# Kernel tuning notes

Hardware: AMD Instinct MI355X
Metric: run time of the kernel (lower is better)

Reference implementation:

```python
import jax, jax.numpy as jnp
import numpy as np

LOG_2PI = float(np.log(2.0 * np.pi))
LOSS_BETA = 1.0
SIGMA = 1.0
EPS = 1e-6


def setup_inputs() -> dict:
    key = jax.random.key(0)
    z_activations = jax.random.normal(key, (2048, 16, 8), dtype=jnp.float32)
    return {"z_activations": z_activations}


def reference(z_activations):
    N, num_attr, pose_dim = z_activations.shape
    x = z_activations.reshape(N, -1)  # (N, K)
    K = x.shape[1]

    # standardize (torch.std is unbiased, ddof=1)
    mean = jnp.mean(x, axis=0, keepdims=True)
    std = jnp.std(x, axis=0, keepdims=True, ddof=1)
    x = (x - mean) / (std + EPS)

    logN = jnp.log(jnp.asarray(N, dtype=x.dtype))

    # per-dimension pairwise squared differences: (N, N, K)
    d = (x[:, None, :] - x[None, :, :]) ** 2

    # joint: log p(x_i | x_j) for K-dim Gaussian, sigma=1
    sq_dist = jnp.sum(d, axis=2)  # (N, N)
    c_joint = -0.5 * K * LOG_2PI - K * jnp.log(jnp.asarray(SIGMA, dtype=x.dtype))
    log_prob_joint = c_joint - sq_dist / (2.0 * SIGMA ** 2)
    log_q_z_given_x = jax.nn.logsumexp(log_prob_joint, axis=1) - logN  # (N,)

    # marginals: 1-D Gaussian per dim, all K at once (fuses the torch K-loop)
    c_marg = -0.5 * LOG_2PI - jnp.log(jnp.asarray(SIGMA, dtype=x.dtype))
    log_prob_marg = c_marg - d / (2.0 * SIGMA ** 2)  # (N, N, K)
    log_q_z_j = jax.nn.logsumexp(log_prob_marg, axis=1) - logN  # (N, K)
    sum_log_q_z_j = jnp.sum(log_q_z_j, axis=1)  # (N,)

    tc_loss = jnp.mean(log_q_z_given_x - sum_log_q_z_j)
    return tc_loss * LOSS_BETA
```

## Files before the change

kernel.cpp:

```cpp
#include <hip/hip_runtime.h>
#include <hip/hip_bf16.h>

#define NROWS 2048
#define KDIM  128
#define NCELL 16
#define PORD  10
#define NJBLK 512

typedef float f32x4  __attribute__((ext_vector_type(4)));
typedef short bf16x8 __attribute__((ext_vector_type(8)));

__device__ __forceinline__ float fexp2(float x){ return __builtin_amdgcn_exp2f(x); }
__device__ __forceinline__ float flog2(float x){ return __builtin_amdgcn_logf(x); }

#define CS 0.8493218002880191f

#define OFF_PART   0
#define OFF_ACCUM  8192
#define OFF_JOINT  8448
#define OFF_SLOG   10496
#define OFF_MOM    12544
#define OFF_CTR    33024
#define OFF_XS     33028
#define ZERO_BASE  OFF_JOINT
#define ZERO_LEN   (2048 + 2048 + 20480 + 4)

__device__ __forceinline__ void col_stats_from(float s, float s2, float& scale, float& shift){
  float m = s * (1.f / NROWS);
  float var = fmaxf((s2 - (float)NROWS * m * m) * (1.f / (NROWS - 1)), 0.f);
  scale = 1.f / (sqrtf(var) + 1e-6f);
  shift = -m * scale;
}

__global__ __launch_bounds__(1024) void tc_stats(const float* __restrict__ x,
                                                 float* __restrict__ ws){
  const int t  = threadIdx.x;
  const int k  = t & 127;
  const int rg = t >> 7;
  const int r0 = blockIdx.x * 64;
  {
    int idx = blockIdx.x * 1024 + t;
    if (idx < ZERO_LEN) ws[ZERO_BASE + idx] = 0.f;
  }
  float s = 0.f, s2 = 0.f;
  #pragma unroll
  for (int it = 0; it < 8; ++it){
    float v = x[(size_t)(r0 + it * 8 + rg) * KDIM + k];
    s += v;
    s2 = fmaf(v, v, s2);
  }
  __shared__ float ls[8][128], ls2[8][128];
  ls[rg][k] = s; ls2[rg][k] = s2;
  __syncthreads();
  if (t < 128){
    float a = 0.f, b = 0.f;
    #pragma unroll
    for (int g = 0; g < 8; ++g){ a += ls[g][t]; b += ls2[g][t]; }
    ws[OFF_PART + blockIdx.x * 256 + t]       = a;
    ws[OFF_PART + blockIdx.x * 256 + 128 + t] = b;
  }
}

__global__ __launch_bounds__(128) void tc_moments(const float* __restrict__ x,
                                                  float* __restrict__ ws){
  const int k   = blockIdx.x >> 4;
  const int seg = blockIdx.x & 15;
  const int t   = threadIdx.x;
  __shared__ float lm[NCELL * PORD];
  lm[t] = 0.f;
  if (t < 32) lm[128 + t] = 0.f;

  float s = 0.f, s2 = 0.f;
  #pragma unroll
  for (int b = 0; b < 32; ++b){
    s  += ws[OFF_PART + b * 256 + k];
    s2 += ws[OFF_PART + b * 256 + 128 + k];
  }
  if (seg == 0 && t == 0){
    ws[OFF_ACCUM + k]       = s;
    ws[OFF_ACCUM + 128 + k] = s2;
  }
  float scale, shift; col_stats_from(s, s2, scale, shift);
  __syncthreads();

  const int row = seg * 128 + t;
  float y = fmaf(x[(size_t)row * KDIM + k], scale, shift);

  {
    __hip_bfloat16 hb = __float2bfloat16(y * CS);
    ((unsigned short*)(ws + OFF_XS))[(size_t)row * KDIM + k] = *(unsigned short*)&hb;
  }

  int c = (int)floorf(y * 2.f + 8.f);
  c = min(max(c, 0), NCELL - 1);
  float u = y - (-3.75f + 0.5f * (float)c);
  float* b10 = &lm[c * PORD];
  atomicAdd(&b10[0], 1.f);
  float pw = u;
  atomicAdd(&b10[1], pw);
  pw *= u; atomicAdd(&b10[2], pw * 0.5f);
  pw *= u; atomicAdd(&b10[3], pw * 1.6666666666e-1f);
  pw *= u; atomicAdd(&b10[4], pw * 4.1666666666e-2f);
  pw *= u; atomicAdd(&b10[5], pw * 8.3333333333e-3f);
  pw *= u; atomicAdd(&b10[6], pw * 1.3888888889e-3f);
  pw *= u; atomicAdd(&b10[7], pw * 1.9841269841e-4f);
  pw *= u; atomicAdd(&b10[8], pw * 2.4801587302e-5f);
  pw *= u; atomicAdd(&b10[9], pw * 2.7557319224e-6f);
  __syncthreads();

  float* mom = ws + OFF_MOM;
  for (int idx = t; idx < NCELL * PORD; idx += 128){
    int c2 = idx / PORD, m = idx - c2 * PORD;
    atomicAdd(&mom[(size_t)(c2 * KDIM + k) * PORD + m], lm[idx]);
  }
}

__global__ __launch_bounds__(512) void tc_joint(const float* __restrict__ x,
                                                float* __restrict__ ws,
                                                float* __restrict__ out){
  __shared__ __align__(16) char ls[49152];
  __shared__ float nI[128], nJ[64];
  __shared__ float red2[8];
  __shared__ int lastflag;

  const int t = threadIdx.x;
  const int wave = t >> 6, lane = t & 63;
  const int bid = blockIdx.x;
  const int bi = bid >> 5, bj = bid & 31;
  const int Ibase = bi * 128, Jbase = bj * 64;
  float* joint = ws + OFF_JOINT;
  float* slog  = ws + OFF_SLOG;
  const float* accum = ws + OFF_ACCUM;
  const float* mom   = ws + OFF_MOM;
  const unsigned short* xs = (const unsigned short*)(ws + OFF_XS);

  #pragma unroll
  for (int q = 0; q < 4; ++q){
    int g = t + q * 512;
    int row = g >> 4, c16 = g & 15;
    uint4 v = *(const uint4*)(xs + (size_t)(Ibase + row) * KDIM + c16 * 8);
    *(uint4*)(ls + row * 256 + ((c16 * 16) ^ ((row & 7) << 4))) = v;
  }
  #pragma unroll
  for (int q = 0; q < 2; ++q){
    int g = t + q * 512;
    int row = g >> 4, c16 = g & 15;
    uint4 v = *(const uint4*)(xs + (size_t)(Jbase + row) * KDIM + c16 * 8);
    *(uint4*)(ls + 32768 + row * 256 + ((c16 * 16) ^ ((row & 7) << 4))) = v;
  }
  __syncthreads();

  if (t < 192){
    int row = (t < 128) ? t : (t - 128);
    const char* base = (t < 128) ? ls : (ls + 32768);
    float n = 0.f;
    #pragma unroll
    for (int g2 = 0; g2 < 16; ++g2){
      uint4 v = *(const uint4*)(base + row * 256 + ((g2 * 16) ^ ((row & 7) << 4)));
      const unsigned int* u = (const unsigned int*)&v;
      #pragma unroll
      for (int e = 0; e < 4; ++e){
        float lo = __builtin_bit_cast(float, u[e] << 16);
        float hi = __builtin_bit_cast(float, u[e] & 0xFFFF0000u);
        n = fmaf(lo, lo, n); n = fmaf(hi, hi, n);
      }
    }
    if (t < 128) nI[row] = n; else nJ[row] = n;
  }
  __syncthreads();

  const int wi = wave >> 2, wj = wave & 3;
  const int mrow0 = wi * 64 + (lane & 15);
  const int nrow  = wj * 16 + (lane & 15);
  f32x4 acc0 = {0.f,0.f,0.f,0.f}, acc1 = acc0, acc2 = acc0, acc3 = acc0;
  #pragma unroll
  for (int kq = 0; kq < 4; ++kq){
    const int boff = kq * 64 + (lane >> 4) * 16;
    const int mx = (mrow0 & 7) << 4;
    bf16x8 bf = *(const bf16x8*)(ls + 32768 + nrow * 256 + (boff ^ ((nrow & 7) << 4)));
    bf16x8 a0 = *(const bf16x8*)(ls + (mrow0 +  0) * 256 + (boff ^ mx));
    bf16x8 a1 = *(const bf16x8*)(ls + (mrow0 + 16) * 256 + (boff ^ mx));
    bf16x8 a2 = *(const bf16x8*)(ls + (mrow0 + 32) * 256 + (boff ^ mx));
    bf16x8 a3 = *(const bf16x8*)(ls + (mrow0 + 48) * 256 + (boff ^ mx));
    acc0 = __builtin_amdgcn_mfma_f32_16x16x32_bf16(a0, bf, acc0, 0, 0, 0);
    acc1 = __builtin_amdgcn_mfma_f32_16x16x32_bf16(a1, bf, acc1, 0, 0, 0);
    acc2 = __builtin_amdgcn_mfma_f32_16x16x32_bf16(a2, bf, acc2, 0, 0, 0);
    acc3 = __builtin_amdgcn_mfma_f32_16x16x32_bf16(a3, bf, acc3, 0, 0, 0);
  }

  const float njv = nJ[nrow];
  const int rbase = (lane >> 4) * 4;
  float jp[4][4];
  #pragma unroll
  for (int mt = 0; mt < 4; ++mt){
    f32x4 a4 = (mt == 0) ? acc0 : (mt == 1) ? acc1 : (mt == 2) ? acc2 : acc3;
    #pragma unroll
    for (int p = 0; p < 4; ++p){
      int iloc = wi * 64 + mt * 16 + rbase + p;
      float pd = nI[iloc] + njv - 2.f * a4[p];
      jp[mt][p] = fexp2(-pd);
    }
  }
  #pragma unroll
  for (int mt = 0; mt < 4; ++mt){
    #pragma unroll
    for (int p = 0; p < 4; ++p){
      float v = jp[mt][p];
      v += __shfl_xor(v, 1); v += __shfl_xor(v, 2);
      v += __shfl_xor(v, 4); v += __shfl_xor(v, 8);
      jp[mt][p] = v;
    }
  }
  if ((lane & 15) == 0){
    #pragma unroll
    for (int mt = 0; mt < 4; ++mt)
      #pragma unroll
      for (int p = 0; p < 4; ++p)
        atomicAdd(&joint[Ibase + wi * 64 + mt * 16 + rbase + p], jp[mt][p]);
  }

  {
    const int k  = t & 127;
    const int ir = t >> 7;
    const int r  = bid * 4 + ir;
    float scale, shift;
    col_stats_from(accum[k], accum[128 + k], scale, shift);
    const float y = fmaf(x[(size_t)r * KDIM + k], scale, shift);
    float S = 0.f;
    #pragma unroll
    for (int c = 0; c < NCELL; ++c){
      const float* mp = mom + (size_t)(c * KDIM + k) * PORD;
      float q0 = mp[0], q1 = mp[1], q2 = mp[2], q3 = mp[3], q4 = mp[4];
      float q5 = mp[5], q6 = mp[6], q7 = mp[7], q8 = mp[8], q9 = mp[9];
      float sC  = y - (-3.75f + 0.5f * (float)c);
      float scl = sC * CS;
      float e  = fexp2(-(scl * scl));
      float prev = 1.f, cur = sC, nxt;
      float inner = fmaf(q1, sC, q0);
      nxt = fmaf(sC, cur, -1.f * prev); inner = fmaf(q2, nxt, inner); prev = cur; cur = nxt;
      nxt = fmaf(sC, cur, -2.f * prev); inner = fmaf(q3, nxt, inner); prev = cur; cur = nxt;
      nxt = fmaf(sC, cur, -3.f * prev); inner = fmaf(q4, nxt, inner); prev = cur; cur = nxt;
      nxt = fmaf(sC, cur, -4.f * prev); inner = fmaf(q5, nxt, inner); prev = cur; cur = nxt;
      nxt = fmaf(sC, cur, -5.f * prev); inner = fmaf(q6, nxt, inner); prev = cur; cur = nxt;
      nxt = fmaf(sC, cur, -6.f * prev); inner = fmaf(q7, nxt, inner); prev = cur; cur = nxt;
      nxt = fmaf(sC, cur, -7.f * prev); inner = fmaf(q8, nxt, inner); prev = cur; cur = nxt;
      nxt = fmaf(sC, cur, -8.f * prev); inner = fmaf(q9, nxt, inner);
      S = fmaf(e, inner, S);
    }
    float lg = flog2(S);
    #pragma unroll
    for (int off = 1; off < 64; off <<= 1) lg += __shfl_xor(lg, off);
    if (lane == 0) atomicAdd(&slog[r], lg);
  }

  __syncthreads();
  if (t == 0){
    __threadfence();
    unsigned int* ctr = (unsigned int*)(ws + OFF_CTR);
    unsigned int old = __hip_atomic_fetch_add(ctr, 1u, __ATOMIC_ACQ_REL, __HIP_MEMORY_SCOPE_AGENT);
    lastflag = (old == NJBLK - 1);
  }
  __syncthreads();
  if (lastflag){
    float acc = 0.f;
    #pragma unroll
    for (int q = 0; q < 4; ++q){
      int r = q * 512 + t;
      float jv = __hip_atomic_load(&joint[r], __ATOMIC_RELAXED, __HIP_MEMORY_SCOPE_AGENT);
      float sv = __hip_atomic_load(&slog[r],  __ATOMIC_RELAXED, __HIP_MEMORY_SCOPE_AGENT);
      acc += 0.6931471805599453f * (flog2(jv) - sv);
    }
    #pragma unroll
    for (int m = 1; m < 64; m <<= 1) acc += __shfl_xor(acc, m);
    if (lane == 0) red2[wave] = acc;
    __syncthreads();
    if (t == 0){
      float tot = 0.f;
      #pragma unroll
      for (int w = 0; w < 8; ++w) tot += red2[w];
      out[0] = tot * (1.0f / NROWS) + 968.32661124224364f;
    }
  }
}

extern "C" void kernel_launch(void* const* d_in, const int* in_sizes, int n_in,
                              void* d_out, int out_size, void* d_ws, size_t ws_size,
                              hipStream_t stream){
  const float* x = (const float*)d_in[0];
  float* out = (float*)d_out;
  float* ws  = (float*)d_ws;
  tc_stats  <<<32, 1024, 0, stream>>>(x, ws);
  tc_moments<<<KDIM * 16, 128, 0, stream>>>(x, ws);
  tc_joint  <<<NJBLK, 512, 0, stream>>>(x, ws, out);
}
```

Baseline: 124.1 us.

## Split joint kernel into separate GEMM and marginal blocks, precompute row norms

```diff
diff --git a/kernel.cpp b/kernel.cpp
--- a/kernel.cpp
+++ b/kernel.cpp
@@ -5,7 +5,9 @@
 #define KDIM  128
 #define NCELL 16
 #define PORD  10
-#define NJBLK 512
+#define MOMS  12
+#define NJ_TILES 512
+#define NBLK_K3 1024
 
 typedef float f32x4  __attribute__((ext_vector_type(4)));
 typedef short bf16x8 __attribute__((ext_vector_type(8)));
@@ -19,11 +21,12 @@
 #define OFF_ACCUM  8192
 #define OFF_JOINT  8448
 #define OFF_SLOG   10496
-#define OFF_MOM    12544
-#define OFF_CTR    33024
-#define OFF_XS     33028
+#define OFF_NRM    12544
+#define OFF_MOM    14592
+#define OFF_CTR    39168
+#define OFF_XS     39172
 #define ZERO_BASE  OFF_JOINT
-#define ZERO_LEN   (2048 + 2048 + 20480 + 4)
+#define ZERO_LEN   (2048 + 2048 + 2048 + 24576 + 4)
 
 __device__ __forceinline__ void col_stats_from(float s, float s2, float& scale, float& shift){
   float m = s * (1.f / NROWS);
@@ -88,7 +91,10 @@
 
   {
     __hip_bfloat16 hb = __float2bfloat16(y * CS);
-    ((unsigned short*)(ws + OFF_XS))[(size_t)row * KDIM + k] = *(unsigned short*)&hb;
+    unsigned short us = *(unsigned short*)&hb;
+    ((unsigned short*)(ws + OFF_XS))[(size_t)row * KDIM + k] = us;
+    float ybf = __builtin_bit_cast(float, (unsigned int)us << 16);
+    atomicAdd(&ws[OFF_NRM + row], ybf * ybf);
   }
 
   int c = (int)floorf(y * 2.f + 8.f);
@@ -111,140 +117,102 @@
   float* mom = ws + OFF_MOM;
   for (int idx = t; idx < NCELL * PORD; idx += 128){
     int c2 = idx / PORD, m = idx - c2 * PORD;
-    atomicAdd(&mom[(size_t)(c2 * KDIM + k) * PORD + m], lm[idx]);
+    atomicAdd(&mom[(size_t)(k * NCELL + c2) * MOMS + m], lm[idx]);
   }
 }
 
 __global__ __launch_bounds__(512) void tc_joint(const float* __restrict__ x,
                                                 float* __restrict__ ws,
                                                 float* __restrict__ out){
-  __shared__ __align__(16) char ls[49152];
-  __shared__ float nI[128], nJ[64];
   __shared__ float red2[8];
   __shared__ int lastflag;
-
   const int t = threadIdx.x;
   const int wave = t >> 6, lane = t & 63;
   const int bid = blockIdx.x;
-  const int bi = bid >> 5, bj = bid & 31;
-  const int Ibase = bi * 128, Jbase = bj * 64;
   float* joint = ws + OFF_JOINT;
   float* slog  = ws + OFF_SLOG;
+  const float* nrm   = ws + OFF_NRM;
   const float* accum = ws + OFF_ACCUM;
   const float* mom   = ws + OFF_MOM;
   const unsigned short* xs = (const unsigned short*)(ws + OFF_XS);
 
-  #pragma unroll
-  for (int q = 0; q < 4; ++q){
-    int g = t + q * 512;
-    int row = g >> 4, c16 = g & 15;
-    uint4 v = *(const uint4*)(xs + (size_t)(Ibase + row) * KDIM + c16 * 8);
-    *(uint4*)(ls + row * 256 + ((c16 * 16) ^ ((row & 7) << 4))) = v;
-  }
-  #pragma unroll
-  for (int q = 0; q < 2; ++q){
-    int g = t + q * 512;
-    int row = g >> 4, c16 = g & 15;
-    uint4 v = *(const uint4*)(xs + (size_t)(Jbase + row) * KDIM + c16 * 8);
-    *(uint4*)(ls + 32768 + row * 256 + ((c16 * 16) ^ ((row & 7) << 4))) = v;
-  }
-  __syncthreads();
-
-  if (t < 192){
-    int row = (t < 128) ? t : (t - 128);
-    const char* base = (t < 128) ? ls : (ls + 32768);
-    float n = 0.f;
-    #pragma unroll
-    for (int g2 = 0; g2 < 16; ++g2){
-      uint4 v = *(const uint4*)(base + row * 256 + ((g2 * 16) ^ ((row & 7) << 4)));
-      const unsigned int* u = (const unsigned int*)&v;
+  if (bid < NJ_TILES){
+    const int bi = bid >> 5, bj = bid & 31;
+    const int Ibase = bi * 128, Jbase = bj * 64;
+    const int wi = wave >> 2, wj = wave & 3;
+    const int lr = lane & 15, hs = lane >> 4;
+
+    f32x4 acc0 = {0.f,0.f,0.f,0.f}, acc1 = acc0, acc2 = acc0, acc3 = acc0;
+    #pragma unroll
+    for (int kq = 0; kq < 4; ++kq){
+      const int co = kq * 32 + hs * 8;
+      bf16x8 bf = *(const bf16x8*)(xs + (size_t)(Jbase + wj * 16 + lr) * KDIM + co);
+      bf16x8 a0 = *(const bf16x8*)(xs + (size_t)(Ibase + wi * 64 + lr +  0) * KDIM + co);
+      bf16x8 a1 = *(const bf16x8*)(xs + (size_t)(Ibase + wi * 64 + lr + 16) * KDIM + co);
+      bf16x8 a2 = *(const bf16x8*)(xs + (size_t)(Ibase + wi * 64 + lr + 32) * KDIM + co);
+      bf16x8 a3 = *(const bf16x8*)(xs + (size_t)(Ibase + wi * 64 + lr + 48) * KDIM + co);
+      acc0 = __builtin_amdgcn_mfma_f32_16x16x32_bf16(a0, bf, acc0, 0, 0, 0);
+      acc1 = __builtin_amdgcn_mfma_f32_16x16x32_bf16(a1, bf, acc1, 0, 0, 0);
+      acc2 = __builtin_amdgcn_mfma_f32_16x16x32_bf16(a2, bf, acc2, 0, 0, 0);
+      acc3 = __builtin_amdgcn_mfma_f32_16x16x32_bf16(a3, bf, acc3, 0, 0, 0);
+    }
+
+    const float njv = nrm[Jbase + wj * 16 + lr];
+    const int rbase = hs * 4;
+    float jp[4][4];
+    #pragma unroll
+    for (int mt = 0; mt < 4; ++mt){
+      f32x4 a4 = (mt == 0) ? acc0 : (mt == 1) ? acc1 : (mt == 2) ? acc2 : acc3;
+      const float4 nI4 = *(const float4*)(nrm + Ibase + wi * 64 + mt * 16 + rbase);
+      jp[mt][0] = fexp2(-(nI4.x + njv - 2.f * a4[0]));
+      jp[mt][1] = fexp2(-(nI4.y + njv - 2.f * a4[1]));
+      jp[mt][2] = fexp2(-(nI4.z + njv - 2.f * a4[2]));
+      jp[mt][3] = fexp2(-(nI4.w + njv - 2.f * a4[3]));
+    }
+    #pragma unroll
+    for (int mt = 0; mt < 4; ++mt){
       #pragma unroll
-      for (int e = 0; e < 4; ++e){
-        float lo = __builtin_bit_cast(float, u[e] << 16);
-        float hi = __builtin_bit_cast(float, u[e] & 0xFFFF0000u);
-        n = fmaf(lo, lo, n); n = fmaf(hi, hi, n);
+      for (int p = 0; p < 4; ++p){
+        float v = jp[mt][p];
+        v += __shfl_xor(v, 1); v += __shfl_xor(v, 2);
+        v += __shfl_xor(v, 4); v += __shfl_xor(v, 8);
+        jp[mt][p] = v;
       }
     }
-    if (t < 128) nI[row] = n; else nJ[row] = n;
-  }
-  __syncthreads();
-
-  const int wi = wave >> 2, wj = wave & 3;
-  const int mrow0 = wi * 64 + (lane & 15);
-  const int nrow  = wj * 16 + (lane & 15);
-  f32x4 acc0 = {0.f,0.f,0.f,0.f}, acc1 = acc0, acc2 = acc0, acc3 = acc0;
-  #pragma unroll
-  for (int kq = 0; kq < 4; ++kq){
-    const int boff = kq * 64 + (lane >> 4) * 16;
-    const int mx = (mrow0 & 7) << 4;
-    bf16x8 bf = *(const bf16x8*)(ls + 32768 + nrow * 256 + (boff ^ ((nrow & 7) << 4)));
-    bf16x8 a0 = *(const bf16x8*)(ls + (mrow0 +  0) * 256 + (boff ^ mx));
-    bf16x8 a1 = *(const bf16x8*)(ls + (mrow0 + 16) * 256 + (boff ^ mx));
-    bf16x8 a2 = *(const bf16x8*)(ls + (mrow0 + 32) * 256 + (boff ^ mx));
-    bf16x8 a3 = *(const bf16x8*)(ls + (mrow0 + 48) * 256 + (boff ^ mx));
-    acc0 = __builtin_amdgcn_mfma_f32_16x16x32_bf16(a0, bf, acc0, 0, 0, 0);
-    acc1 = __builtin_amdgcn_mfma_f32_16x16x32_bf16(a1, bf, acc1, 0, 0, 0);
-    acc2 = __builtin_amdgcn_mfma_f32_16x16x32_bf16(a2, bf, acc2, 0, 0, 0);
-    acc3 = __builtin_amdgcn_mfma_f32_16x16x32_bf16(a3, bf, acc3, 0, 0, 0);
-  }
-
-  const float njv = nJ[nrow];
-  const int rbase = (lane >> 4) * 4;
-  float jp[4][4];
-  #pragma unroll
-  for (int mt = 0; mt < 4; ++mt){
-    f32x4 a4 = (mt == 0) ? acc0 : (mt == 1) ? acc1 : (mt == 2) ? acc2 : acc3;
-    #pragma unroll
-    for (int p = 0; p < 4; ++p){
-      int iloc = wi * 64 + mt * 16 + rbase + p;
-      float pd = nI[iloc] + njv - 2.f * a4[p];
-      jp[mt][p] = fexp2(-pd);
-    }
-  }
-  #pragma unroll
-  for (int mt = 0; mt < 4; ++mt){
-    #pragma unroll
-    for (int p = 0; p < 4; ++p){
-      float v = jp[mt][p];
-      v += __shfl_xor(v, 1); v += __shfl_xor(v, 2);
-      v += __shfl_xor(v, 4); v += __shfl_xor(v, 8);
-      jp[mt][p] = v;
-    }
-  }
-  if ((lane & 15) == 0){
-    #pragma unroll
-    for (int mt = 0; mt < 4; ++mt)
+    if (lr == 0){
       #pragma unroll
-      for (int p = 0; p < 4; ++p)
-        atomicAdd(&joint[Ibase + wi * 64 + mt * 16 + rbase + p], jp[mt][p]);
-  }
-
-  {
+      for (int mt = 0; mt < 4; ++mt)
+        #pragma unroll
+        for (int p = 0; p < 4; ++p)
+          atomicAdd(&joint[Ibase + wi * 64 + mt * 16 + rbase + p], jp[mt][p]);
+    }
+  } else {
     const int k  = t & 127;
     const int ir = t >> 7;
-    const int r  = bid * 4 + ir;
+    const int r  = (bid - NJ_TILES) * 4 + ir;
     float scale, shift;
     col_stats_from(accum[k], accum[128 + k], scale, shift);
     const float y = fmaf(x[(size_t)r * KDIM + k], scale, shift);
     float S = 0.f;
     #pragma unroll
     for (int c = 0; c < NCELL; ++c){
-      const float* mp = mom + (size_t)(c * KDIM + k) * PORD;
-      float q0 = mp[0], q1 = mp[1], q2 = mp[2], q3 = mp[3], q4 = mp[4];
-      float q5 = mp[5], q6 = mp[6], q7 = mp[7], q8 = mp[8], q9 = mp[9];
+      const float* mp = mom + (size_t)(k * NCELL + c) * MOMS;
+      const float4 v0 = *(const float4*)(mp);
+      const float4 v1 = *(const float4*)(mp + 4);
+      const float4 v2 = *(const float4*)(mp + 8);
       float sC  = y - (-3.75f + 0.5f * (float)c);
       float scl = sC * CS;
       float e  = fexp2(-(scl * scl));
       float prev = 1.f, cur = sC, nxt;
-      float inner = fmaf(q1, sC, q0);
-      nxt = fmaf(sC, cur, -1.f * prev); inner = fmaf(q2, nxt, inner); prev = cur; cur = nxt;
-      nxt = fmaf(sC, cur, -2.f * prev); inner = fmaf(q3, nxt, inner); prev = cur; cur = nxt;
-      nxt = fmaf(sC, cur, -3.f * prev); inner = fmaf(q4, nxt, inner); prev = cur; cur = nxt;
-      nxt = fmaf(sC, cur, -4.f * prev); inner = fmaf(q5, nxt, inner); prev = cur; cur = nxt;
-      nxt = fmaf(sC, cur, -5.f * prev); inner = fmaf(q6, nxt, inner); prev = cur; cur = nxt;
-      nxt = fmaf(sC, cur, -6.f * prev); inner = fmaf(q7, nxt, inner); prev = cur; cur = nxt;
-      nxt = fmaf(sC, cur, -7.f * prev); inner = fmaf(q8, nxt, inner); prev = cur; cur = nxt;
-      nxt = fmaf(sC, cur, -8.f * prev); inner = fmaf(q9, nxt, inner);
+      float inner = fmaf(v0.y, sC, v0.x);
+      nxt = fmaf(sC, cur, -1.f * prev); inner = fmaf(v0.z, nxt, inner); prev = cur; cur = nxt;
+      nxt = fmaf(sC, cur, -2.f * prev); inner = fmaf(v0.w, nxt, inner); prev = cur; cur = nxt;
+      nxt = fmaf(sC, cur, -3.f * prev); inner = fmaf(v1.x, nxt, inner); prev = cur; cur = nxt;
+      nxt = fmaf(sC, cur, -4.f * prev); inner = fmaf(v1.y, nxt, inner); prev = cur; cur = nxt;
+      nxt = fmaf(sC, cur, -5.f * prev); inner = fmaf(v1.z, nxt, inner); prev = cur; cur = nxt;
+      nxt = fmaf(sC, cur, -6.f * prev); inner = fmaf(v1.w, nxt, inner); prev = cur; cur = nxt;
+      nxt = fmaf(sC, cur, -7.f * prev); inner = fmaf(v2.x, nxt, inner); prev = cur; cur = nxt;
+      nxt = fmaf(sC, cur, -8.f * prev); inner = fmaf(v2.y, nxt, inner);
       S = fmaf(e, inner, S);
     }
     float lg = flog2(S);
@@ -258,7 +226,7 @@
     __threadfence();
     unsigned int* ctr = (unsigned int*)(ws + OFF_CTR);
     unsigned int old = __hip_atomic_fetch_add(ctr, 1u, __ATOMIC_ACQ_REL, __HIP_MEMORY_SCOPE_AGENT);
-    lastflag = (old == NJBLK - 1);
+    lastflag = (old == NBLK_K3 - 1);
   }
   __syncthreads();
   if (lastflag){
@@ -291,5 +259,5 @@
   float* ws  = (float*)d_ws;
   tc_stats  <<<32, 1024, 0, stream>>>(x, ws);
   tc_moments<<<KDIM * 16, 128, 0, stream>>>(x, ws);
-  tc_joint  <<<NJBLK, 512, 0, stream>>>(x, ws, out);
-}
+  tc_joint  <<<NBLK_K3, 512, 0, stream>>>(x, ws, out);
+}
```

Result: slower. 166.6 us (+34.3%).
